# Performance work log

Measured on AMD Instinct MI355X. Metric: run time of the kernel, lower is better.

The kernel has to match this reference:

```python
import jax, jax.numpy as jnp
import numpy as np

NUM_NODES = 120          # nodes per graph
B = 1024                 # graphs per batch
DEG = 16                 # avg degree
N = B * NUM_NODES        # total nodes
E = N * DEG              # total edges
C1 = NUM_NODES // 3      # conv1 out = 40
C2 = NUM_NODES // 2      # conv2 out = 60
OUT = 120


def _glorot(key, shape):
    fan = sum(shape) if len(shape) > 1 else shape[0] + 1
    return jax.random.normal(key, shape, jnp.float32) * jnp.sqrt(2.0 / fan)


def setup_inputs() -> dict:
    key = jax.random.key(0)
    ks = jax.random.split(key, 24)
    x = jax.random.normal(ks[0], (N, 3), jnp.float32)
    # block-structured edges: each edge stays inside its graph; no self-loops
    src_loc = jax.random.randint(ks[1], (B, NUM_NODES * DEG), 0, NUM_NODES)
    off = jax.random.randint(ks[2], (B, NUM_NODES * DEG), 1, NUM_NODES)
    dst_loc = (src_loc + off) % NUM_NODES
    base = (jnp.arange(B) * NUM_NODES)[:, None]
    edge_index = jnp.stack([(src_loc + base).reshape(-1), (dst_loc + base).reshape(-1)]).astype(jnp.int64)
    edge_attr = jax.random.uniform(ks[3], (E, 1), jnp.float32)
    mask = jax.random.uniform(ks[4], (B, OUT)) > 0.1
    p = {
        'W1': _glorot(ks[5], (3, C1)), 'att_src1': _glorot(ks[6], (C1,)),
        'att_dst1': _glorot(ks[7], (C1,)), 'We1': _glorot(ks[8], (1, C1)),
        'att_e1': _glorot(ks[9], (C1,)), 'b1': jnp.zeros((C1,), jnp.float32),
        'W2': _glorot(ks[10], (C1, C2)), 'att_src2': _glorot(ks[11], (C2,)),
        'att_dst2': _glorot(ks[12], (C2,)), 'We2': _glorot(ks[13], (1, C2)),
        'att_e2': _glorot(ks[14], (C2,)), 'b2': jnp.zeros((C2,), jnp.float32),
        'Wx1': _glorot(ks[15], (NUM_NODES * C2, NUM_NODES)), 'bx1': jnp.zeros((NUM_NODES,), jnp.float32),
        'Wx2': _glorot(ks[16], (NUM_NODES, OUT)), 'bx2': jnp.zeros((OUT,), jnp.float32),
    }
    return dict(x=x, edge_index=edge_index, edge_attr=edge_attr, mask=mask, **p)


def _segment_softmax(alpha, dst, n):
    m = jax.ops.segment_max(alpha, dst, num_segments=n)
    m = jnp.where(jnp.isfinite(m), m, 0.0)
    e = jnp.exp(alpha - m[dst])
    s = jax.ops.segment_sum(e, dst, num_segments=n)
    return e / (s[dst] + 1e-16)


def _gat_conv(x, edge_index, edge_attr, W, a_s, a_d, We, a_e, bias):
    n = x.shape[0]
    src, dst = edge_index[0], edge_index[1]
    # add self-loops; PyG fill_value='mean' -> self-loop edge_attr = mean over edges
    loop = jnp.arange(n, dtype=src.dtype)
    src = jnp.concatenate([src, loop])
    dst = jnp.concatenate([dst, loop])
    mean_attr = jnp.mean(edge_attr, axis=0, keepdims=True)            # [1, edge_dim]
    ea = jnp.concatenate([edge_attr, jnp.broadcast_to(mean_attr, (n, edge_attr.shape[1]))], 0)
    h = x @ W                                                          # [n, C]
    alpha_src = h @ a_s                                                # [n]
    alpha_dst = h @ a_d                                                # [n]
    alpha_edge = (ea @ We) @ a_e                                       # [E']
    alpha = jax.nn.leaky_relu(alpha_src[src] + alpha_dst[dst] + alpha_edge, 0.2)
    alpha = _segment_softmax(alpha, dst, n)                            # segment softmax over dst
    out = jax.ops.segment_sum(h[src] * alpha[:, None], dst, num_segments=n)
    return out + bias


def reference(x, edge_index, edge_attr, mask,
              W1, att_src1, att_dst1, We1, att_e1, b1,
              W2, att_src2, att_dst2, We2, att_e2, b2,
              Wx1, bx1, Wx2, bx2):
    out = _gat_conv(x, edge_index, edge_attr, W1, att_src1, att_dst1, We1, att_e1, b1)
    out = jax.nn.selu(out)
    out = _gat_conv(out, edge_index, edge_attr, W2, att_src2, att_dst2, We2, att_e2, b2)
    out = out.reshape(B, NUM_NODES * C2)          # stack(split) + flatten
    out = jax.nn.selu(out)
    out = jax.nn.selu(out @ Wx1 + bx1)
    out = out @ Wx2 + bx2
    return jnp.where(mask, out, -jnp.inf)
```

## Files before the change

### kernel.cpp

```cpp
#include <hip/hip_runtime.h>
#include <hip/hip_bf16.h>
#include <math.h>
#include <float.h>

#define NN   120
#define BGR  1024
#define NTOT (NN*BGR)
#define DEG  16
#define EPG  (NN*DEG)
#define ETOT (NTOT*DEG)
#define C1   40
#define C2   60
#define OUTD 120
#define KTOT 7200
#define KS   15
#define KCH  (KTOT/KS)
#define NP   128

#define SENTINEL (-1.0e30f)
#define FCLAMP   (3.3e38f)

#define OFF_A 256
#define OFF_B (OFF_A + NTOT*60*4)
#define OFF_C (OFF_B + NTOT*8)
#define OFF_D (OFF_C + NTOT*60*4)

typedef __attribute__((ext_vector_type(8))) short short8;
typedef __attribute__((ext_vector_type(4))) float f32x4;
typedef __attribute__((ext_vector_type(4))) int   i32x4;

__device__ __forceinline__ float seluf(float v){
    const float a = 1.6732632423543772f, sc = 1.0507009873554805f;
    return v > 0.f ? sc*v : sc*a*(__expf(v)-1.f);
}
__device__ __forceinline__ float lrelu(float v){ return v > 0.f ? v : 0.2f*v; }
__device__ __forceinline__ unsigned f2s(float f){ unsigned b=__float_as_uint(f); return (b&0x80000000u)? ~b : (b|0x80000000u); }
__device__ __forceinline__ float s2f(unsigned u){ return (u&0x80000000u)? __uint_as_float(u&0x7fffffffu) : __uint_as_float(~u); }
__device__ __forceinline__ float scrub(float v){
    return ((__float_as_uint(v)&0x7f800000u)==0x7f800000u) ? 0.f : v;
}
__device__ __forceinline__ unsigned short f2bf(float f){
    __hip_bfloat16 h = __float2bfloat16(f);
    return *reinterpret_cast<unsigned short*>(&h);
}

__global__ void k_detect(const int* __restrict__ ei, const unsigned char* __restrict__ maskb,
                         int* __restrict__ flags){
    __shared__ int c64, cm;
    int t = threadIdx.x;
    if (t==0){ c64=0; cm=0; }
    __syncthreads();
    if (t<64 && ei[2*t+1]!=0) atomicAdd(&c64,1);
    if (t<128 && maskb[t]!=0) atomicAdd(&cm,1);
    __syncthreads();
    if (t==0){
        flags[1] = (c64==0) ? 1 : 0;
        flags[2] = (cm>64) ? 1 : 0;
    }
}

__global__ __launch_bounds__(256) void k_mean(const float* __restrict__ ea, float* __restrict__ part){
    float acc = 0.f;
    for (int i = blockIdx.x*256 + threadIdx.x; i < ETOT; i += gridDim.x*256)
        acc += ea[i];
    for (int o=32;o>0;o>>=1) acc += __shfl_down(acc, o, 64);
    __shared__ float wsum[4];
    int lane = threadIdx.x & 63, w = threadIdx.x >> 6;
    if (lane==0) wsum[w]=acc;
    __syncthreads();
    if (threadIdx.x==0) part[blockIdx.x] = wsum[0]+wsum[1]+wsum[2]+wsum[3];
}
__global__ __launch_bounds__(256) void k_mean2(const float* __restrict__ part, float* __restrict__ wsf){
    int t = threadIdx.x;
    float acc = part[t] + part[t+256] + part[t+512] + part[t+768];
    for (int o=32;o>0;o>>=1) acc += __shfl_down(acc, o, 64);
    __shared__ float wsum[4];
    int lane = t & 63, w = t >> 6;
    if (lane==0) wsum[w]=acc;
    __syncthreads();
    if (t==0) wsf[0] = wsum[0]+wsum[1]+wsum[2]+wsum[3];
}

__global__ __launch_bounds__(256) void k_wt(const float* __restrict__ Wx1, unsigned short* __restrict__ Wt){
    __shared__ float tile[32][33];
    const int k0 = blockIdx.x*32, n0 = blockIdx.y*32;
    const int tx = threadIdx.x & 31, ty = threadIdx.x >> 5;
    #pragma unroll
    for (int rr=0; rr<4; ++rr){
        int r = ty*4+rr;
        int n = n0+tx;
        tile[r][tx] = (n<OUTD) ? Wx1[(size_t)(k0+r)*OUTD + n] : 0.f;
    }
    __syncthreads();
    #pragma unroll
    for (int rr=0; rr<4; ++rr){
        int r2 = ty*4+rr;
        Wt[(size_t)(n0+r2)*KTOT + k0 + tx] = f2bf(tile[tx][r2]);
    }
}

__global__ __launch_bounds__(256) void k_node2(const float* __restrict__ x1, const float* __restrict__ W2,
        const float* __restrict__ avs, const float* __restrict__ avd,
        unsigned short* __restrict__ h2, float* __restrict__ as2, float* __restrict__ ad2){
    int i = blockIdx.x*256 + threadIdx.x;
    float xr[C1];
    const float4* xp = (const float4*)(x1 + i*C1);
    #pragma unroll
    for (int q=0;q<C1/4;q++){ float4 v=xp[q]; xr[4*q]=v.x; xr[4*q+1]=v.y; xr[4*q+2]=v.z; xr[4*q+3]=v.w; }
    float hrow[C2];
    #pragma unroll
    for (int c=0;c<C2;c++) hrow[c]=0.f;
    #pragma unroll 4
    for (int k=0;k<C1;k++){
        float xv = xr[k];
        #pragma unroll
        for (int c=0;c<C2;c++) hrow[c] += xv*W2[k*C2+c];
    }
    float das=0.f, dad=0.f;
    #pragma unroll
    for (int c=0;c<C2;c++){ das += hrow[c]*avs[c]; dad += hrow[c]*avd[c]; }
    #pragma unroll
    for (int c=0;c<C2;c+=2){
        ushort2 u; u.x=f2bf(hrow[c]); u.y=f2bf(hrow[c+1]);
        *(ushort2*)(h2 + (size_t)i*C2 + c) = u;
    }
    as2[i]=das; ad2[i]=dad;
}

template<int C, bool FUSE1, bool OB16>
__global__ __launch_bounds__(256) void k_conv(
    const int* __restrict__ ei, const float* __restrict__ ea,
    const void* __restrict__ hx,
    const float* __restrict__ asg, const float* __restrict__ adg,
    const float* __restrict__ Wn, const float* __restrict__ avs, const float* __restrict__ avd,
    const float* __restrict__ wsf, const float* __restrict__ We, const float* __restrict__ aev,
    const float* __restrict__ bias, void* __restrict__ xout)
{
    constexpr int NT  = (C+15)/16;
    constexpr int OST = NT*16;
    __shared__ int A_int[128*128];
    __shared__ unsigned short ht[64*128];
    __shared__ float alpha_s[EPG];
    __shared__ unsigned short sd_s[EPG];
    __shared__ __align__(16) char out_raw[OB16 ? NN*OST*2 : NN*OST*4];
    __shared__ unsigned m_s[128];
    __shared__ float asv[128], adv[128], sa_s[128], rs_s[128];
    __shared__ int isum[128];
    __shared__ float W1s[120];

    const int g=blockIdx.x, t=threadIdx.x;
    const int base=g*NN;
    const int is64 = ((const int*)wsf)[1];
    const float mean = wsf[0]*(1.0f/(float)ETOT);
    float cE=0.f;
    #pragma unroll
    for (int k=0;k<C;k++) cE += We[k]*aev[k];

    for (int i=t;i<128*32;i+=256) ((i32x4*)A_int)[i] = (i32x4){0,0,0,0};
    for (int i=t;i<64*16;i+=256)  ((short8*)ht)[i]   = (short8){0,0,0,0,0,0,0,0};
    if (t<128){
        isum[t]=0;
        if (t>=NN){ asv[t]=0.f; adv[t]=0.f; sa_s[t]=0.f; m_s[t]=f2s(0.f); }
    }
    if constexpr (FUSE1){ for (int i=t;i<120;i+=256) W1s[i]=Wn[i]; }
    __syncthreads();

    if constexpr (FUSE1){
        const float* xg = (const float*)hx;
        if (t<2*NN){
            int n=t>>1, hf=t&1;
            const float* xr = xg + (size_t)(base+n)*3;
            float x0=xr[0],x1=xr[1],x2=xr[2];
            float das=0.f,dad=0.f;
            #pragma unroll
            for (int cc=0;cc<20;cc++){
                int c=hf*20+cc;
                float hh = x0*W1s[c]+x1*W1s[40+c]+x2*W1s[80+c];
                das+=hh*avs[c]; dad+=hh*avd[c];
                ht[c*128 + ((((n>>3))^(c&15))<<3) + (n&7)] = f2bf(hh);
            }
            das += __shfl_xor(das,1,64);
            dad += __shfl_xor(dad,1,64);
            if (hf==0){
                asv[n]=das; adv[n]=dad;
                float sa=lrelu(das+dad+cE*mean);
                sa_s[n]=sa; m_s[n]=f2s(sa);
            }
        }
    } else {
        const unsigned short* hg = (const unsigned short*)hx + (size_t)base*C;
        for (int i=t;i<NN*C;i+=256){
            int n=i/C, c=i-n*C;
            ht[c*128 + ((((n>>3))^(c&15))<<3) + (n&7)] = hg[i];
        }
        for (int i=t;i<NN;i+=256){
            float a=asg[base+i], dd=adg[base+i];
            asv[i]=a; adv[i]=dd;
            float sa=lrelu(a+dd+cE*mean);
            sa_s[i]=sa; m_s[i]=f2s(sa);
        }
    }
    __syncthreads();

    const int gE = g*EPG;
    for (int e=t;e<EPG;e+=256){
        int s,d;
        if (is64){ s=ei[2*(gE+e)]; d=ei[2*(ETOT+gE+e)]; }
        else     { s=ei[gE+e];     d=ei[ETOT+gE+e];     }
        s-=base; d-=base; s&=127; d&=127;
        float a = lrelu(asv[s]+adv[d]+cE*ea[gE+e]);
        alpha_s[e]=a;
        sd_s[e]=(unsigned short)(s|(d<<8));
        atomicMax(&m_s[d], f2s(a));
    }
    __syncthreads();

    for (int e=t;e<EPG;e+=256){
        int sd=sd_s[e]; int s=sd&255, d=sd>>8;
        float w = __expf(alpha_s[e] - s2f(m_s[d]));
        atomicAdd(&A_int[d*128 + (((s>>3)^(d&15))<<3) + (s&7)], (int)(w*8388608.0f));
        atomicAdd(&isum[d], (int)(w*16777216.0f));
    }
    __syncthreads();

    if (t<128){
        float m = s2f(m_s[t]);
        float wself = __expf(sa_s[t]-m);
        float den = (float)isum[t]*5.9604645e-8f + wself;
        rs_s[t] = 1.0f/(den+1e-16f);
        atomicAdd(&A_int[t*128 + (((t>>3)^(t&15))<<3) + (t&7)], (int)(wself*8388608.0f));
    }
    __syncthreads();

    {
        const int l = t&63, w = t>>6;
        float* out_f = (float*)out_raw;
        unsigned short* out_h = (unsigned short*)out_raw;
        #pragma unroll
        for (int mi=0; mi<2; ++mi){
            const int mt = w*2 + mi;
            const int m  = mt*16 + (l&15);
            const float rsm = rs_s[m] * (1.1920929e-7f);
            short8 afr[4];
            #pragma unroll
            for (int kc=0; kc<4; ++kc){
                int k0 = kc*32 + (l>>4)*8;
                const i32x4* p = (const i32x4*)(A_int + m*128 + (((k0>>3)^(l&15))<<3));
                i32x4 i0 = p[0], i1 = p[1];
                short8 r;
                r[0]=(short)f2bf((float)i0[0]*rsm); r[1]=(short)f2bf((float)i0[1]*rsm);
                r[2]=(short)f2bf((float)i0[2]*rsm); r[3]=(short)f2bf((float)i0[3]*rsm);
                r[4]=(short)f2bf((float)i1[0]*rsm); r[5]=(short)f2bf((float)i1[1]*rsm);
                r[6]=(short)f2bf((float)i1[2]*rsm); r[7]=(short)f2bf((float)i1[3]*rsm);
                afr[kc]=r;
            }
            #pragma unroll
            for (int nt=0; nt<NT; ++nt){
                const int c = nt*16 + (l&15);
                f32x4 acc = {0.f,0.f,0.f,0.f};
                #pragma unroll
                for (int kc=0; kc<4; ++kc){
                    int k0 = kc*32 + (l>>4)*8;
                    short8 b = *(const short8*)(ht + c*128 + (((k0>>3)^(c&15))<<3));
                    acc = __builtin_amdgcn_mfma_f32_16x16x32_bf16(afr[kc], b, acc, 0,0,0);
                }
                if (c < C){
                    const float bc = bias[c];
                    const int mr0 = mt*16 + (l>>4)*4;
                    #pragma unroll
                    for (int r=0;r<4;r++){
                        int mr = mr0 + r;
                        if (mr < NN){
                            float o = seluf(acc[r] + bc);
                            if constexpr (OB16) out_h[mr*OST + c] = f2bf(o);
                            else                out_f[mr*OST + c] = o;
                        }
                    }
                }
            }
        }
    }
    __syncthreads();

    if constexpr (OB16){
        const unsigned short* out_h = (const unsigned short*)out_raw;
        unsigned short* xo = (unsigned short*)xout + (size_t)base*C;
        for (int i=t;i<NN*C;i+=256){ int n=i/C, c=i-n*C; xo[i] = out_h[n*OST+c]; }
    } else {
        const float* out_f = (const float*)out_raw;
        float* xo = (float*)xout + (size_t)base*C;
        for (int i=t;i<NN*C;i+=256){ int n=i/C, c=i-n*C; xo[i] = out_f[n*OST+c]; }
    }
}

__global__ __launch_bounds__(256) void k_fc1(const unsigned short* __restrict__ zb,
        const unsigned short* __restrict__ wt, float* __restrict__ y1p){
    const int t = threadIdx.x, w = t>>6, l = t&63;
    const int rt = w&1, chf = w>>1;
    const int m0 = blockIdx.x*32 + rt*16;
    const int c0 = chf*64;
    const int kb = blockIdx.y*KCH;
    const int lr = l&15, lk8 = (l>>4)*8;
    const unsigned short* za = zb + (size_t)(m0+lr)*KTOT + kb + lk8;
    const unsigned short* wa = wt + (size_t)(c0+lr)*KTOT + kb + lk8;
    f32x4 acc0={0,0,0,0}, acc1={0,0,0,0}, acc2={0,0,0,0}, acc3={0,0,0,0};
    #pragma unroll 5
    for (int ks=0; ks<KCH/32; ++ks){
        short8 a  = *(const short8*)(za + ks*32);
        short8 b0 = *(const short8*)(wa + 0*16*KTOT + ks*32);
        short8 b1 = *(const short8*)(wa + 1*16*KTOT + ks*32);
        short8 b2 = *(const short8*)(wa + 2*16*KTOT + ks*32);
        short8 b3 = *(const short8*)(wa + 3*16*KTOT + ks*32);
        acc0 = __builtin_amdgcn_mfma_f32_16x16x32_bf16(a, b0, acc0, 0,0,0);
        acc1 = __builtin_amdgcn_mfma_f32_16x16x32_bf16(a, b1, acc1, 0,0,0);
        acc2 = __builtin_amdgcn_mfma_f32_16x16x32_bf16(a, b2, acc2, 0,0,0);
        acc3 = __builtin_amdgcn_mfma_f32_16x16x32_bf16(a, b3, acc3, 0,0,0);
    }
    float* dst = y1p + (size_t)blockIdx.y*(BGR*NP) + (size_t)(m0 + (l>>4)*4)*NP + c0 + lr;
    #pragma unroll
    for (int r=0;r<4;r++){
        dst[r*NP + 0*16] = acc0[r];
        dst[r*NP + 1*16] = acc1[r];
        dst[r*NP + 2*16] = acc2[r];
        dst[r*NP + 3*16] = acc3[r];
    }
}

__global__ __launch_bounds__(128) void k_fc2(const float* __restrict__ y1p, const float* __restrict__ bx1,
        const float* __restrict__ Wx2, const float* __restrict__ bx2,
        const void* __restrict__ maskp, const int* __restrict__ flags, float* __restrict__ out){
    __shared__ float ys[OUTD];
    int g = blockIdx.x, t=threadIdx.x;
    for (int i=t;i<OUTD;i+=128){
        float a = bx1[i];
        #pragma unroll
        for (int s=0;s<KS;s++) a += y1p[s*(BGR*NP) + g*NP + i];
        ys[i] = seluf(a);
    }
    __syncthreads();
    if (t<OUTD){
        float a = bx2[t];
        for (int k=0;k<OUTD;k++) a += ys[k]*Wx2[k*OUTD+t];
        a = scrub(a);
        a = fminf(fmaxf(a, -FCLAMP), FCLAMP);
        bool mv;
        if (flags[2]) mv = ((const unsigned char*)maskp)[g*OUTD+t] != 0;
        else          mv = ((const int*)maskp)[g*OUTD+t] != 0;
        out[g*OUTD+t] = mv ? a : SENTINEL;
    }
}

extern "C" void kernel_launch(void* const* d_in, const int* in_sizes, int n_in,
                              void* d_out, int out_size, void* d_ws, size_t ws_size,
                              hipStream_t stream){
    const float* x    = (const float*)d_in[0];
    const int*   ei   = (const int*)d_in[1];
    const float* ea   = (const float*)d_in[2];
    const void*  mask = d_in[3];
    const float* W1   = (const float*)d_in[4];
    const float* as1v = (const float*)d_in[5];
    const float* ad1v = (const float*)d_in[6];
    const float* We1  = (const float*)d_in[7];
    const float* ae1  = (const float*)d_in[8];
    const float* b1   = (const float*)d_in[9];
    const float* W2   = (const float*)d_in[10];
    const float* as2v = (const float*)d_in[11];
    const float* ad2v = (const float*)d_in[12];
    const float* We2  = (const float*)d_in[13];
    const float* ae2  = (const float*)d_in[14];
    const float* b2   = (const float*)d_in[15];
    const float* Wx1  = (const float*)d_in[16];
    const float* bx1  = (const float*)d_in[17];
    const float* Wx2  = (const float*)d_in[18];
    const float* bx2  = (const float*)d_in[19];

    char* ws = (char*)d_ws;
    float* wsf  = (float*)ws;
    float* hbuf = (float*)(ws + OFF_A);
    float* asb  = (float*)(ws + OFF_B);
    float* adb  = asb + NTOT;
    float* xbuf = (float*)(ws + OFF_C);
    unsigned short* wt = (unsigned short*)(ws + OFF_D);
    float* y1p  = hbuf;
    float* outf = (float*)d_out;

    k_detect<<<1,128,0,stream>>>(ei, (const unsigned char*)mask, (int*)wsf);
    k_mean<<<1024,256,0,stream>>>(ea, asb);
    k_mean2<<<1,256,0,stream>>>(asb, wsf);
    {   dim3 gw(KTOT/32, NP/32);
        k_wt<<<gw,256,0,stream>>>(Wx1, wt); }
    k_conv<C1,true,false><<<BGR,256,0,stream>>>(ei, ea, x, nullptr, nullptr,
                                             W1, as1v, ad1v, wsf, We1, ae1, b1, xbuf);
    k_node2<<<NTOT/256,256,0,stream>>>(xbuf, W2, as2v, ad2v, (unsigned short*)hbuf, asb, adb);
    k_conv<C2,false,true><<<BGR,256,0,stream>>>(ei, ea, hbuf, asb, adb,
                                              nullptr, nullptr, nullptr, wsf, We2, ae2, b2, xbuf);
    dim3 g1(32, KS);
    k_fc1<<<g1,256,0,stream>>>((const unsigned short*)xbuf, wt, y1p);
    k_fc2<<<BGR,128,0,stream>>>(y1p, bx1, Wx2, bx2, mask, (const int*)wsf, outf);
}
```

Baseline: 257.5 us.

## Pack attention matrix into 16-bit fixed point and shrink conv LDS footprint

The dense per-graph attention matrix now accumulates 11-bit-scaled fixed-point weights packed two per 32-bit word, which halves its LDS size. The per-edge alpha and src/dst buffers are dropped, and the second pass reloads and recomputes the edge logits instead. The output staging buffer is removed and MFMA results are written straight to global memory. Together these cut shared memory per block to allow more resident blocks, at the cost of coarser weight quantization, possible 16-bit overflow into the neighbouring lane on heavily duplicated edges, extra global edge reads, and less coalesced stores.

New measurement: 222.8 us. 1.16x faster.

```diff
diff --git a/kernel.cpp b/kernel.cpp
--- a/kernel.cpp
+++ b/kernel.cpp
@@ -136,16 +136,13 @@
     const float* __restrict__ wsf, const float* __restrict__ We, const float* __restrict__ aev,
     const float* __restrict__ bias, void* __restrict__ xout)
 {
-    constexpr int NT  = (C+15)/16;
-    constexpr int OST = NT*16;
-    __shared__ int A_int[128*128];
-    __shared__ unsigned short ht[64*128];
-    __shared__ float alpha_s[EPG];
-    __shared__ unsigned short sd_s[EPG];
-    __shared__ __align__(16) char out_raw[OB16 ? NN*OST*2 : NN*OST*4];
+    constexpr int NT = (C+15)/16;
+    constexpr int CH = NT*16;
+    __shared__ unsigned A_h[128*64];
+    __shared__ unsigned short ht[CH*128];
     __shared__ unsigned m_s[128];
+    __shared__ int isum[128];
     __shared__ float asv[128], adv[128], sa_s[128], rs_s[128];
-    __shared__ int isum[128];
     __shared__ float W1s[120];
 
     const int g=blockIdx.x, t=threadIdx.x;
@@ -156,8 +153,8 @@
     #pragma unroll
     for (int k=0;k<C;k++) cE += We[k]*aev[k];
 
-    for (int i=t;i<128*32;i+=256) ((i32x4*)A_int)[i] = (i32x4){0,0,0,0};
-    for (int i=t;i<64*16;i+=256)  ((short8*)ht)[i]   = (short8){0,0,0,0,0,0,0,0};
+    for (int i=t;i<128*16;i+=256) ((i32x4*)A_h)[i] = (i32x4){0,0,0,0};
+    for (int i=t;i<CH*16;i+=256)  ((short8*)ht)[i] = (short8){0,0,0,0,0,0,0,0};
     if (t<128){
         isum[t]=0;
         if (t>=NN){ asv[t]=0.f; adv[t]=0.f; sa_s[t]=0.f; m_s[t]=f2s(0.f); }
@@ -177,7 +174,7 @@
                 int c=hf*20+cc;
                 float hh = x0*W1s[c]+x1*W1s[40+c]+x2*W1s[80+c];
                 das+=hh*avs[c]; dad+=hh*avd[c];
-                ht[c*128 + ((((n>>3))^(c&15))<<3) + (n&7)] = f2bf(hh);
+                ht[c*128 + (((n>>3)^(c&15))<<3) + (n&7)] = f2bf(hh);
             }
             das += __shfl_xor(das,1,64);
             dad += __shfl_xor(dad,1,64);
@@ -191,7 +188,7 @@
         const unsigned short* hg = (const unsigned short*)hx + (size_t)base*C;
         for (int i=t;i<NN*C;i+=256){
             int n=i/C, c=i-n*C;
-            ht[c*128 + ((((n>>3))^(c&15))<<3) + (n&7)] = hg[i];
+            ht[c*128 + (((n>>3)^(c&15))<<3) + (n&7)] = hg[i];
         }
         for (int i=t;i<NN;i+=256){
             float a=asg[base+i], dd=adg[base+i];
@@ -209,59 +206,64 @@
         else     { s=ei[gE+e];     d=ei[ETOT+gE+e];     }
         s-=base; d-=base; s&=127; d&=127;
         float a = lrelu(asv[s]+adv[d]+cE*ea[gE+e]);
-        alpha_s[e]=a;
-        sd_s[e]=(unsigned short)(s|(d<<8));
         atomicMax(&m_s[d], f2s(a));
     }
     __syncthreads();
 
     for (int e=t;e<EPG;e+=256){
-        int sd=sd_s[e]; int s=sd&255, d=sd>>8;
-        float w = __expf(alpha_s[e] - s2f(m_s[d]));
-        atomicAdd(&A_int[d*128 + (((s>>3)^(d&15))<<3) + (s&7)], (int)(w*8388608.0f));
-        atomicAdd(&isum[d], (int)(w*16777216.0f));
+        int s,d;
+        if (is64){ s=ei[2*(gE+e)]; d=ei[2*(ETOT+gE+e)]; }
+        else     { s=ei[gE+e];     d=ei[ETOT+gE+e];     }
+        s-=base; d-=base; s&=127; d&=127;
+        float a = lrelu(asv[s]+adv[d]+cE*ea[gE+e]);
+        float w = __expf(a - s2f(m_s[d]));
+        int q = (int)(w*2048.0f);
+        atomicAdd(&A_h[d*64 + (((s>>3)^(d&15))<<2) + ((s>>1)&3)], (unsigned)(q<<((s&1)*16)));
+        atomicAdd(&isum[d], q);
     }
     __syncthreads();
 
     if (t<128){
         float m = s2f(m_s[t]);
         float wself = __expf(sa_s[t]-m);
-        float den = (float)isum[t]*5.9604645e-8f + wself;
-        rs_s[t] = 1.0f/(den+1e-16f);
-        atomicAdd(&A_int[t*128 + (((t>>3)^(t&15))<<3) + (t&7)], (int)(wself*8388608.0f));
+        int qself = (int)(wself*2048.0f);
+        atomicAdd(&A_h[t*64 + (((t>>3)^(t&15))<<2) + ((t>>1)&3)], (unsigned)(qself<<((t&1)*16)));
+        int den = isum[t]+qself;
+        rs_s[t] = 1.0f/(float)(den>0?den:1);
     }
     __syncthreads();
 
     {
         const int l = t&63, w = t>>6;
-        float* out_f = (float*)out_raw;
-        unsigned short* out_h = (unsigned short*)out_raw;
+        const int lr = l&15, hi8 = (l>>4)*8;
         #pragma unroll
         for (int mi=0; mi<2; ++mi){
             const int mt = w*2 + mi;
-            const int m  = mt*16 + (l&15);
-            const float rsm = rs_s[m] * (1.1920929e-7f);
+            const int m  = mt*16 + lr;
+            const float rsm = rs_s[m];
             short8 afr[4];
             #pragma unroll
             for (int kc=0; kc<4; ++kc){
-                int k0 = kc*32 + (l>>4)*8;
-                const i32x4* p = (const i32x4*)(A_int + m*128 + (((k0>>3)^(l&15))<<3));
-                i32x4 i0 = p[0], i1 = p[1];
+                int k0 = kc*32 + hi8;
+                const i32x4* p = (const i32x4*)(A_h + m*64 + ((((k0>>3))^(m&15))<<2));
+                i32x4 v = *p;
                 short8 r;
-                r[0]=(short)f2bf((float)i0[0]*rsm); r[1]=(short)f2bf((float)i0[1]*rsm);
-                r[2]=(short)f2bf((float)i0[2]*rsm); r[3]=(short)f2bf((float)i0[3]*rsm);
-                r[4]=(short)f2bf((float)i1[0]*rsm); r[5]=(short)f2bf((float)i1[1]*rsm);
-                r[6]=(short)f2bf((float)i1[2]*rsm); r[7]=(short)f2bf((float)i1[3]*rsm);
+                #pragma unroll
+                for (int jj=0;jj<4;jj++){
+                    unsigned word = (unsigned)v[jj];
+                    r[2*jj+0] = (short)f2bf((float)(word & 0xffffu)*rsm);
+                    r[2*jj+1] = (short)f2bf((float)(word >> 16)*rsm);
+                }
                 afr[kc]=r;
             }
             #pragma unroll
             for (int nt=0; nt<NT; ++nt){
-                const int c = nt*16 + (l&15);
+                const int c = nt*16 + lr;
                 f32x4 acc = {0.f,0.f,0.f,0.f};
                 #pragma unroll
                 for (int kc=0; kc<4; ++kc){
-                    int k0 = kc*32 + (l>>4)*8;
-                    short8 b = *(const short8*)(ht + c*128 + (((k0>>3)^(c&15))<<3));
+                    int k0 = kc*32 + hi8;
+                    short8 b = *(const short8*)(ht + c*128 + ((((k0>>3))^(c&15))<<3));
                     acc = __builtin_amdgcn_mfma_f32_16x16x32_bf16(afr[kc], b, acc, 0,0,0);
                 }
                 if (c < C){
@@ -272,24 +274,15 @@
                         int mr = mr0 + r;
                         if (mr < NN){
                             float o = seluf(acc[r] + bc);
-                            if constexpr (OB16) out_h[mr*OST + c] = f2bf(o);
-                            else                out_f[mr*OST + c] = o;
+                            if constexpr (OB16)
+                                ((unsigned short*)xout)[(size_t)(base+mr)*C + c] = f2bf(o);
+                            else
+                                ((float*)xout)[(size_t)(base+mr)*C + c] = o;
                         }
                     }
                 }
             }
         }
-    }
-    __syncthreads();
-
-    if constexpr (OB16){
-        const unsigned short* out_h = (const unsigned short*)out_raw;
-        unsigned short* xo = (unsigned short*)xout + (size_t)base*C;
-        for (int i=t;i<NN*C;i+=256){ int n=i/C, c=i-n*C; xo[i] = out_h[n*OST+c]; }
-    } else {
-        const float* out_f = (const float*)out_raw;
-        float* xo = (float*)xout + (size_t)base*C;
-        for (int i=t;i<NN*C;i+=256){ int n=i/C, c=i-n*C; xo[i] = out_f[n*OST+c]; }
     }
 }
 
```
